# Kernel optimization log

Measured on AMD Instinct MI355X. Metric: run time of the kernel, lower is better.

## Reference

```python
import jax, jax.numpy as jnp
import numpy as np

HEAD_DIM = 64

def setup_inputs() -> dict:
    key = jax.random.key(0)
    k1, k2, k3, k4 = jax.random.split(key, 4)
    B, T, C, D = 8, 2048, 1024, HEAD_DIM
    x = jax.random.normal(k1, (B, T, C), dtype=jnp.float32)
    Wq = jax.random.normal(k2, (C, D), dtype=jnp.float32) * (1.0 / np.sqrt(C))
    Wk = jax.random.normal(k3, (C, D), dtype=jnp.float32) * (1.0 / np.sqrt(C))
    Wv = jax.random.normal(k4, (C, D), dtype=jnp.float32) * (1.0 / np.sqrt(C))
    return {"x": x, "Wq": Wq, "Wk": Wk, "Wv": Wv}

def reference(x, Wq, Wk, Wv):
    B, T, C = x.shape
    D = Wq.shape[1]
    q = jnp.einsum('btc,cd->btd', x, Wq)
    k = jnp.einsum('btc,cd->btd', x, Wk)
    v = jnp.einsum('btc,cd->btd', x, Wv)
    scale = 1.0 / jnp.sqrt(jnp.asarray(D, dtype=x.dtype))
    wei = jnp.einsum('bqd,bkd->bqk', q, k) * scale  # [B,T,T]
    causal = jnp.tril(jnp.ones((T, T), dtype=bool))
    wei = jnp.where(causal[None, :, :], wei, -jnp.inf)
    wei = jax.nn.softmax(wei, axis=-1)
    # dropout p=0.0 (eval) -> identity
    out = jnp.einsum('bqk,bkd->bqd', wei, v)  # [B,T,D]
    return out
```

## Files before the change

kernel.cpp:

```cpp
#include <hip/hip_runtime.h>
#include <hip/hip_bf16.h>


typedef __attribute__((ext_vector_type(8))) short short8;
typedef __attribute__((ext_vector_type(4))) float f32x4;

#define MFMA16(a, b, c) __builtin_amdgcn_mfma_f32_16x16x32_bf16((a), (b), (c), 0, 0, 0)

__device__ __forceinline__ unsigned short f2bf(float f) {
  unsigned int u = __builtin_bit_cast(unsigned int, f);
  unsigned int r = 0x7fffu + ((u >> 16) & 1u);
  return (unsigned short)((u + r) >> 16);
}

#define BATCH 8
#define SEQ   2048
#define CDIM  1024
#define DDIM  64
#define NTOK  (BATCH * SEQ)
#define LOG2E 1.44269504f

__global__ __launch_bounds__(256) void wt_kernel(const float* __restrict__ Wq,
                                                 const float* __restrict__ Wk,
                                                 const float* __restrict__ Wv,
                                                 unsigned short* __restrict__ WT) {
  int tid = blockIdx.x * 256 + threadIdx.x;
  int c    = tid & 63;
  int rest = tid >> 6;
  int k    = rest & 1023;
  int wi   = rest >> 10;
  const float* W = (wi == 0) ? Wq : ((wi == 1) ? Wk : Wv);
  float v = W[k * DDIM + c];
  if (wi == 0) v *= 0.125f * LOG2E;
  int row  = wi * 64 + c;
  int step = k >> 6;
  int col  = k & 63;
  size_t idx = (size_t)step * 12288 + (size_t)row * 64 +
               (size_t)(((col >> 3) ^ (row & 7)) * 8) + (col & 7);
  WT[idx] = f2bf(v);
}

__global__ __launch_bounds__(512) void proj_kernel(const float* __restrict__ x,
                                                   const unsigned short* __restrict__ WT,
                                                   unsigned short* __restrict__ qws,
                                                   unsigned short* __restrict__ kws,
                                                   unsigned short* __restrict__ vtws) {
  __shared__ __align__(16) unsigned short xs[2][32 * 64];
  __shared__ __align__(16) unsigned short wl[2][192 * 64];

  const int tid  = threadIdx.x;
  const int lane = tid & 63;
  const int w    = tid >> 6;
  const int wm   = w & 1;
  const int wn   = w >> 1;
  const int c16  = lane & 15;
  const int hi   = lane >> 4;
  const int n0   = blockIdx.x * 32;
  const bool xldr = (tid < 256);
  const int trow = (tid >> 3) & 31;
  const int kch  = tid & 7;

  f32x4 acc[3];
#pragma unroll
  for (int ct = 0; ct < 3; ++ct) acc[ct] = (f32x4){0.f, 0.f, 0.f, 0.f};

  const float* xbase = x + (size_t)(n0 + trow) * CDIM + kch * 8;
  const int xsw = trow * 64 + ((kch ^ (trow & 7)) * 8);

  const unsigned short* wsrc = WT + (size_t)w * 1536 + (size_t)lane * 8;
  auto stage_wt = [&](int step, int bufi) {
    const unsigned short* s = wsrc + (size_t)step * 12288;
    unsigned short* d = &wl[bufi][w * 1536];
#pragma unroll
    for (int j = 0; j < 3; ++j)
      __builtin_amdgcn_global_load_lds(
          (const __attribute__((address_space(1))) void*)(s + j * 512),
          (__attribute__((address_space(3))) void*)(d + j * 512), 16, 0, 0);
  };
  auto xstore = [&](f32x4 a, f32x4 b, int bufi) {
    short8 h;
#pragma unroll
    for (int j = 0; j < 4; ++j) { h[j] = (short)f2bf(a[j]); h[4 + j] = (short)f2bf(b[j]); }
    *reinterpret_cast<short8*>(&xs[bufi][xsw]) = h;
  };

  f32x4 xa1 = {0,0,0,0}, xb1 = xa1, xa2 = xa1, xb2 = xa1;
  if (xldr) {
    f32x4 a0 = *reinterpret_cast<const f32x4*>(xbase);
    f32x4 b0 = *reinterpret_cast<const f32x4*>(xbase + 4);
    xstore(a0, b0, 0);
    xa1 = *reinterpret_cast<const f32x4*>(xbase + 64);
    xb1 = *reinterpret_cast<const f32x4*>(xbase + 64 + 4);
  }
  stage_wt(0, 0);
  __syncthreads();

  int cur = 0;
  for (int st = 0; st < 16; ++st) {
    if (st + 2 < 16 && xldr) {
      xa2 = *reinterpret_cast<const f32x4*>(xbase + (st + 2) * 64);
      xb2 = *reinterpret_cast<const f32x4*>(xbase + (st + 2) * 64 + 4);
    }
    if (st + 1 < 16) stage_wt(st + 1, cur ^ 1);

    short8 bfrag[2];
    {
      int r = wm * 16 + c16;
#pragma unroll
      for (int f = 0; f < 2; ++f)
        bfrag[f] = *reinterpret_cast<const short8*>(
            &xs[cur][r * 64 + (((f * 4 + hi) ^ (r & 7)) * 8)]);
    }
#pragma unroll
    for (int ct = 0; ct < 3; ++ct) {
      int ra = (wn * 3 + ct) * 16 + c16;
#pragma unroll
      for (int f = 0; f < 2; ++f) {
        short8 af = *reinterpret_cast<const short8*>(
            &wl[cur][ra * 64 + (((f * 4 + hi) ^ (ra & 7)) * 8)]);
        acc[ct] = MFMA16(af, bfrag[f], acc[ct]);
      }
    }

    if (st + 1 < 16 && xldr) xstore(xa1, xb1, cur ^ 1);
    __syncthreads();
    xa1 = xa2; xb1 = xb2;
    cur ^= 1;
  }

  {
    const int token = n0 + wm * 16 + c16;
    const int b = token >> 11;
    const int t = token & 2047;
#pragma unroll
    for (int ct = 0; ct < 3; ++ct) {
      int cg = (wn * 3 + ct) * 16 + hi * 4;
      unsigned short h[4];
#pragma unroll
      for (int r = 0; r < 4; ++r) h[r] = f2bf(acc[ct][r]);
      if (cg < 64) {
        *reinterpret_cast<ushort4*>(qws + (size_t)token * DDIM + cg) =
            make_ushort4(h[0], h[1], h[2], h[3]);
      } else if (cg < 128) {
        *reinterpret_cast<ushort4*>(kws + (size_t)token * DDIM + (cg - 64)) =
            make_ushort4(h[0], h[1], h[2], h[3]);
      } else {
        int cv = cg - 128;
#pragma unroll
        for (int r = 0; r < 4; ++r)
          vtws[(size_t)(b * DDIM + cv + r) * SEQ + t] = h[r];
      }
    }
  }
}

__global__ __launch_bounds__(256) void attn_partial(const unsigned short* __restrict__ qws,
                                                    const unsigned short* __restrict__ kws,
                                                    const unsigned short* __restrict__ vtws,
                                                    float* __restrict__ po,
                                                    float* __restrict__ pml,
                                                    int MAXCH, int CHUNK) {
  __shared__ __align__(16) unsigned short kt[2][64 * 64];
  __shared__ __align__(16) unsigned short vt[2][64 * 64];
  __shared__ __align__(16) unsigned short pt[4][1024];

  const int id = blockIdx.x;
  const int b  = id & 7;
  const int qt = (id >> 3) & 31;
  const int ch = id >> 8;

  const int kv_end = qt * 64 + 64;
  const int kv0_ch = ch * CHUNK;
  if (kv0_ch >= kv_end) return;
  const int block_lim = min(kv0_ch + CHUNK, kv_end);
  const int nt = (block_lim - kv0_ch + 63) >> 6;

  const int tid  = threadIdx.x;
  const int lane = tid & 63;
  const int w    = tid >> 6;
  const int c    = lane & 15;
  const int hi   = lane >> 4;
  const int qr0  = qt * 64 + w * 16;
  const int q    = qr0 + c;
  const int kv_last = qr0 + 15;

  const unsigned short* qb = qws + (size_t)b * SEQ * DDIM;
  short8 aq0 = *reinterpret_cast<const short8*>(qb + (size_t)q * DDIM + hi * 8);
  short8 aq1 = *reinterpret_cast<const short8*>(qb + (size_t)q * DDIM + 32 + hi * 8);

  float m = -INFINITY, l = 0.f;
  f32x4 o[4];
#pragma unroll
  for (int dn = 0; dn < 4; ++dn) o[dn] = (f32x4){0.f, 0.f, 0.f, 0.f};

  unsigned short* pwv = pt[w];
  const unsigned short* kb = kws + (size_t)b * SEQ * DDIM;
  const unsigned short* vb = vtws + (size_t)b * DDIM * SEQ;

  auto stage_kv = [&](int bufi, int kv0) {
#pragma unroll
    for (int j = 0; j < 2; ++j) {
      int p   = w * 128 + j * 64 + lane;
      int row = p >> 3;
      int chk = (p & 7) ^ (row & 7);
      __builtin_amdgcn_global_load_lds(
          (const __attribute__((address_space(1))) void*)(kb + (size_t)(kv0 + row) * DDIM + chk * 8),
          (__attribute__((address_space(3))) void*)(&kt[bufi][w * 1024 + j * 512]), 16, 0, 0);
      __builtin_amdgcn_global_load_lds(
          (const __attribute__((address_space(1))) void*)(vb + (size_t)row * SEQ + kv0 + chk * 8),
          (__attribute__((address_space(3))) void*)(&vt[bufi][w * 1024 + j * 512]), 16, 0, 0);
    }
  };

  stage_kv(0, kv0_ch);
  asm volatile("s_waitcnt vmcnt(0)" ::: "memory");
  __builtin_amdgcn_s_barrier();

  int cur = 0;
  for (int t = 0; t < nt; ++t) {
    const int kv0 = kv0_ch + t * 64;
    if (t + 1 < nt) stage_kv(cur ^ 1, kv0 + 64);

    if (kv0 <= kv_last) {
      f32x4 s[4];
#pragma unroll
      for (int n = 0; n < 4; ++n) {
        if (kv0 + n * 16 > kv_last) {
          s[n] = (f32x4){-INFINITY, -INFINITY, -INFINITY, -INFINITY};
          continue;
        }
        const unsigned short* kr = &kt[cur][(n * 16 + c) * 64];
        short8 ka0 = *reinterpret_cast<const short8*>(kr + ((hi ^ (c & 7)) * 8));
        short8 ka1 = *reinterpret_cast<const short8*>(kr + (((4 + hi) ^ (c & 7)) * 8));
        f32x4 z = (f32x4){0.f, 0.f, 0.f, 0.f};
        z = MFMA16(ka0, aq0, z);
        s[n] = MFMA16(ka1, aq1, z);
      }

      if (kv0 + 63 > qr0) {
#pragma unroll
        for (int n = 0; n < 4; ++n)
#pragma unroll
          for (int r = 0; r < 4; ++r)
            if (kv0 + n * 16 + hi * 4 + r > q) s[n][r] = -INFINITY;
      }

      float mx = -INFINITY;
#pragma unroll
      for (int n = 0; n < 4; ++n)
        mx = fmaxf(mx, fmaxf(fmaxf(s[n][0], s[n][1]), fmaxf(s[n][2], s[n][3])));
      mx = fmaxf(mx, __shfl_xor(mx, 16, 64));
      mx = fmaxf(mx, __shfl_xor(mx, 32, 64));

      float nm = fmaxf(m, mx);
      float sc = __builtin_exp2f(m - nm);
      m = nm;

      float ssum = 0.f;
#pragma unroll
      for (int n = 0; n < 4; ++n) {
        float pv0 = __builtin_exp2f(s[n][0] - nm);
        float pv1 = __builtin_exp2f(s[n][1] - nm);
        float pv2 = __builtin_exp2f(s[n][2] - nm);
        float pv3 = __builtin_exp2f(s[n][3] - nm);
        ssum += (pv0 + pv1) + (pv2 + pv3);
        ushort4 h4 = make_ushort4(f2bf(pv0), f2bf(pv1), f2bf(pv2), f2bf(pv3));
        *reinterpret_cast<ushort4*>(
            pwv + (2 * n + (hi >> 1)) * 128 + c * 8 + (hi & 1) * 4) = h4;
      }
      ssum += __shfl_xor(ssum, 16, 64);
      ssum += __shfl_xor(ssum, 32, 64);
      l = l * sc + ssum;

#pragma unroll
      for (int dn = 0; dn < 4; ++dn) o[dn] *= sc;

      const int nf = (kv0 + 32 <= kv_last) ? 2 : 1;
      for (int f = 0; f < nf; ++f) {
        short8 bp = *reinterpret_cast<const short8*>(pwv + (f * 4 + hi) * 128 + c * 8);
#pragma unroll
        for (int dn = 0; dn < 4; ++dn) {
          const unsigned short* vr = &vt[cur][(dn * 16 + c) * 64];
          short8 va = *reinterpret_cast<const short8*>(vr + (((f * 4 + hi) ^ (c & 7)) * 8));
          o[dn] = MFMA16(va, bp, o[dn]);
        }
      }
    }

    if (t + 1 < nt) {
      asm volatile("s_waitcnt vmcnt(0)" ::: "memory");
      __builtin_amdgcn_s_barrier();
    }
    cur ^= 1;
  }

  float* pob = po + (((size_t)(b * 32 + qt) * MAXCH + ch) * 64 + w * 16 + c) * 64 + hi * 4;
#pragma unroll
  for (int dn = 0; dn < 4; ++dn)
    *reinterpret_cast<f32x4*>(pob + dn * 16) = o[dn];

  if (hi == 0) {
    *reinterpret_cast<float2*>(
        pml + (((size_t)(b * 32 + qt) * MAXCH + ch) * 64 + w * 16 + c) * 2) =
        make_float2(m, l);
  }
}

__global__ __launch_bounds__(256) void attn_combine(const float* __restrict__ po,
                                                    const float* __restrict__ pml,
                                                    float* __restrict__ out,
                                                    int MAXCH, int CHUNK) {
  const int id = blockIdx.x;
  const int b  = id & 7;
  const int qt = id >> 3;
  const int tid = threadIdx.x;
  const int row = tid >> 2;
  const int cg  = tid & 3;
  const int nch = min((qt * 64 + 64 + CHUNK - 1) / CHUNK, MAXCH);

  const size_t base = (size_t)(b * 32 + qt) * MAXCH;

  float mv0 = -INFINITY, mv1 = -INFINITY, mv2 = -INFINITY, mv3 = -INFINITY;
  float mv4 = -INFINITY, mv5 = -INFINITY, mv6 = -INFINITY, mv7 = -INFINITY;
  float lv0 = 0, lv1 = 0, lv2 = 0, lv3 = 0, lv4 = 0, lv5 = 0, lv6 = 0, lv7 = 0;
#define LOADML(i) if (i < nch) { \
    float2 t = *reinterpret_cast<const float2*>(pml + (base + i) * 128 + row * 2); \
    mv##i = t.x; lv##i = t.y; }
  LOADML(0) LOADML(1) LOADML(2) LOADML(3) LOADML(4) LOADML(5) LOADML(6) LOADML(7)
#undef LOADML

  float M = fmaxf(fmaxf(fmaxf(mv0, mv1), fmaxf(mv2, mv3)),
                  fmaxf(fmaxf(mv4, mv5), fmaxf(mv6, mv7)));

  float L = 0.f;
  f32x4 a0 = {0.f,0.f,0.f,0.f}, a1 = a0, a2 = a0, a3 = a0;
#define ACC(i) if (i < nch) { \
    float wgt = __builtin_exp2f(mv##i - M); \
    L += wgt * lv##i; \
    const float* p = po + (base + i) * 4096 + row * 64 + cg * 16; \
    a0 += wgt * *reinterpret_cast<const f32x4*>(p); \
    a1 += wgt * *reinterpret_cast<const f32x4*>(p + 4); \
    a2 += wgt * *reinterpret_cast<const f32x4*>(p + 8); \
    a3 += wgt * *reinterpret_cast<const f32x4*>(p + 12); }
  ACC(0) ACC(1) ACC(2) ACC(3) ACC(4) ACC(5) ACC(6) ACC(7)
#undef ACC

  float invL = 1.f / L;
  float* ob = out + ((size_t)b * SEQ + qt * 64 + row) * 64 + cg * 16;
  *reinterpret_cast<f32x4*>(ob)      = a0 * invL;
  *reinterpret_cast<f32x4*>(ob + 4)  = a1 * invL;
  *reinterpret_cast<f32x4*>(ob + 8)  = a2 * invL;
  *reinterpret_cast<f32x4*>(ob + 12) = a3 * invL;
}

extern "C" void kernel_launch(void* const* d_in, const int* in_sizes, int n_in,
                              void* d_out, int out_size, void* d_ws, size_t ws_size,
                              hipStream_t stream) {
  const float* x  = (const float*)d_in[0];
  const float* Wq = (const float*)d_in[1];
  const float* Wk = (const float*)d_in[2];
  const float* Wv = (const float*)d_in[3];
  float* out = (float*)d_out;

  unsigned short* qws  = (unsigned short*)d_ws;
  unsigned short* kws  = qws + (size_t)NTOK * DDIM;
  unsigned short* vtws = kws + (size_t)NTOK * DDIM;
  unsigned short* WT   = vtws + (size_t)NTOK * DDIM;
  size_t fixed_end = (size_t)NTOK * DDIM * 3 * 2 + 192 * 1024 * 2;

  int MAXCH = 1;
  {
    const int cand[4] = {8, 4, 2, 1};
    for (int i = 0; i < 4; ++i) {
      size_t need = fixed_end +
                    (size_t)cand[i] * (8ull * 32 * 64 * 64 * 4 + 8ull * 32 * 64 * 2 * 4);
      if (need <= ws_size) { MAXCH = cand[i]; break; }
    }
  }

  wt_kernel<<<768, 256, 0, stream>>>(Wq, Wk, Wv, WT);
  proj_kernel<<<NTOK / 32, 512, 0, stream>>>(x, WT, qws, kws, vtws);

  float* po  = (float*)((char*)d_ws + fixed_end);
  float* pml = po + (size_t)BATCH * 32 * MAXCH * 64 * 64;
  int CHUNK = SEQ / MAXCH;
  attn_partial<<<32 * MAXCH * BATCH, 256, 0, stream>>>(qws, kws, vtws, po, pml,
                                                       MAXCH, CHUNK);
  attn_combine<<<32 * BATCH, 256, 0, stream>>>(po, pml, out, MAXCH, CHUNK);
}
```

Baseline: 55.10 us.

## Load K/V fragments directly from global memory and reverse query-tile order

Removes the LDS double-buffered K/V staging and block barriers, so each wave loads its MFMA operand fragments straight from global memory (relying on L1/L2 caching), and loops only up to its own causal limit. It also reverses query-tile block order so the heaviest causal tiles launch first. This gets rid of barrier synchronisation and LDS traffic, and lets waves skip tiles independently. In exchange, each of the four waves re-reads the same K/V from global/L2 with no software prefetch, which raises cache traffic and can expose memory latency.

```diff
diff --git a/kernel.cpp b/kernel.cpp
--- a/kernel.cpp
+++ b/kernel.cpp
@@ -160,20 +160,17 @@
                                                     float* __restrict__ po,
                                                     float* __restrict__ pml,
                                                     int MAXCH, int CHUNK) {
-  __shared__ __align__(16) unsigned short kt[2][64 * 64];
-  __shared__ __align__(16) unsigned short vt[2][64 * 64];
   __shared__ __align__(16) unsigned short pt[4][1024];
 
   const int id = blockIdx.x;
   const int b  = id & 7;
-  const int qt = (id >> 3) & 31;
+  const int qt = 31 - ((id >> 3) & 31);
   const int ch = id >> 8;
 
   const int kv_end = qt * 64 + 64;
   const int kv0_ch = ch * CHUNK;
   if (kv0_ch >= kv_end) return;
   const int block_lim = min(kv0_ch + CHUNK, kv_end);
-  const int nt = (block_lim - kv0_ch + 63) >> 6;
 
   const int tid  = threadIdx.x;
   const int lane = tid & 63;
@@ -197,101 +194,81 @@
   const unsigned short* kb = kws + (size_t)b * SEQ * DDIM;
   const unsigned short* vb = vtws + (size_t)b * DDIM * SEQ;
 
-  auto stage_kv = [&](int bufi, int kv0) {
-#pragma unroll
-    for (int j = 0; j < 2; ++j) {
-      int p   = w * 128 + j * 64 + lane;
-      int row = p >> 3;
-      int chk = (p & 7) ^ (row & 7);
-      __builtin_amdgcn_global_load_lds(
-          (const __attribute__((address_space(1))) void*)(kb + (size_t)(kv0 + row) * DDIM + chk * 8),
-          (__attribute__((address_space(3))) void*)(&kt[bufi][w * 1024 + j * 512]), 16, 0, 0);
-      __builtin_amdgcn_global_load_lds(
-          (const __attribute__((address_space(1))) void*)(vb + (size_t)row * SEQ + kv0 + chk * 8),
-          (__attribute__((address_space(3))) void*)(&vt[bufi][w * 1024 + j * 512]), 16, 0, 0);
-    }
-  };
-
-  stage_kv(0, kv0_ch);
-  asm volatile("s_waitcnt vmcnt(0)" ::: "memory");
-  __builtin_amdgcn_s_barrier();
-
-  int cur = 0;
-  for (int t = 0; t < nt; ++t) {
-    const int kv0 = kv0_ch + t * 64;
-    if (t + 1 < nt) stage_kv(cur ^ 1, kv0 + 64);
-
-    if (kv0 <= kv_last) {
-      f32x4 s[4];
-#pragma unroll
-      for (int n = 0; n < 4; ++n) {
-        if (kv0 + n * 16 > kv_last) {
-          s[n] = (f32x4){-INFINITY, -INFINITY, -INFINITY, -INFINITY};
-          continue;
-        }
-        const unsigned short* kr = &kt[cur][(n * 16 + c) * 64];
-        short8 ka0 = *reinterpret_cast<const short8*>(kr + ((hi ^ (c & 7)) * 8));
-        short8 ka1 = *reinterpret_cast<const short8*>(kr + (((4 + hi) ^ (c & 7)) * 8));
+  const int lim = min(block_lim, kv_last + 1);
+
+  for (int kv0 = kv0_ch; kv0 < lim; kv0 += 64) {
+    const int nn = min(3, (kv_last - kv0) >> 4);
+
+    short8 ka[4][2];
+#pragma unroll
+    for (int n = 0; n < 4; ++n) {
+      if (n <= nn) {
+        const unsigned short* kr = kb + (size_t)(kv0 + n * 16 + c) * DDIM + hi * 8;
+        ka[n][0] = *reinterpret_cast<const short8*>(kr);
+        ka[n][1] = *reinterpret_cast<const short8*>(kr + 32);
+      }
+    }
+
+    f32x4 s[4];
+#pragma unroll
+    for (int n = 0; n < 4; ++n) {
+      if (n <= nn) {
         f32x4 z = (f32x4){0.f, 0.f, 0.f, 0.f};
-        z = MFMA16(ka0, aq0, z);
-        s[n] = MFMA16(ka1, aq1, z);
-      }
-
-      if (kv0 + 63 > qr0) {
-#pragma unroll
-        for (int n = 0; n < 4; ++n)
-#pragma unroll
-          for (int r = 0; r < 4; ++r)
-            if (kv0 + n * 16 + hi * 4 + r > q) s[n][r] = -INFINITY;
-      }
-
-      float mx = -INFINITY;
+        z = MFMA16(ka[n][0], aq0, z);
+        s[n] = MFMA16(ka[n][1], aq1, z);
+      } else {
+        s[n] = (f32x4){-INFINITY, -INFINITY, -INFINITY, -INFINITY};
+      }
+    }
+
+    if (kv0 + 63 > qr0) {
 #pragma unroll
       for (int n = 0; n < 4; ++n)
-        mx = fmaxf(mx, fmaxf(fmaxf(s[n][0], s[n][1]), fmaxf(s[n][2], s[n][3])));
-      mx = fmaxf(mx, __shfl_xor(mx, 16, 64));
-      mx = fmaxf(mx, __shfl_xor(mx, 32, 64));
-
-      float nm = fmaxf(m, mx);
-      float sc = __builtin_exp2f(m - nm);
-      m = nm;
-
-      float ssum = 0.f;
-#pragma unroll
-      for (int n = 0; n < 4; ++n) {
-        float pv0 = __builtin_exp2f(s[n][0] - nm);
-        float pv1 = __builtin_exp2f(s[n][1] - nm);
-        float pv2 = __builtin_exp2f(s[n][2] - nm);
-        float pv3 = __builtin_exp2f(s[n][3] - nm);
-        ssum += (pv0 + pv1) + (pv2 + pv3);
-        ushort4 h4 = make_ushort4(f2bf(pv0), f2bf(pv1), f2bf(pv2), f2bf(pv3));
-        *reinterpret_cast<ushort4*>(
-            pwv + (2 * n + (hi >> 1)) * 128 + c * 8 + (hi & 1) * 4) = h4;
-      }
-      ssum += __shfl_xor(ssum, 16, 64);
-      ssum += __shfl_xor(ssum, 32, 64);
-      l = l * sc + ssum;
-
-#pragma unroll
-      for (int dn = 0; dn < 4; ++dn) o[dn] *= sc;
-
-      const int nf = (kv0 + 32 <= kv_last) ? 2 : 1;
-      for (int f = 0; f < nf; ++f) {
-        short8 bp = *reinterpret_cast<const short8*>(pwv + (f * 4 + hi) * 128 + c * 8);
-#pragma unroll
-        for (int dn = 0; dn < 4; ++dn) {
-          const unsigned short* vr = &vt[cur][(dn * 16 + c) * 64];
-          short8 va = *reinterpret_cast<const short8*>(vr + (((f * 4 + hi) ^ (c & 7)) * 8));
-          o[dn] = MFMA16(va, bp, o[dn]);
-        }
-      }
-    }
-
-    if (t + 1 < nt) {
-      asm volatile("s_waitcnt vmcnt(0)" ::: "memory");
-      __builtin_amdgcn_s_barrier();
-    }
-    cur ^= 1;
+#pragma unroll
+        for (int r = 0; r < 4; ++r)
+          if (kv0 + n * 16 + hi * 4 + r > q) s[n][r] = -INFINITY;
+    }
+
+    float mx = -INFINITY;
+#pragma unroll
+    for (int n = 0; n < 4; ++n)
+      mx = fmaxf(mx, fmaxf(fmaxf(s[n][0], s[n][1]), fmaxf(s[n][2], s[n][3])));
+    mx = fmaxf(mx, __shfl_xor(mx, 16, 64));
+    mx = fmaxf(mx, __shfl_xor(mx, 32, 64));
+
+    float nm = fmaxf(m, mx);
+    float sc = __builtin_exp2f(m - nm);
+    m = nm;
+
+    float ssum = 0.f;
+#pragma unroll
+    for (int n = 0; n < 4; ++n) {
+      float pv0 = __builtin_exp2f(s[n][0] - nm);
+      float pv1 = __builtin_exp2f(s[n][1] - nm);
+      float pv2 = __builtin_exp2f(s[n][2] - nm);
+      float pv3 = __builtin_exp2f(s[n][3] - nm);
+      ssum += (pv0 + pv1) + (pv2 + pv3);
+      ushort4 h4 = make_ushort4(f2bf(pv0), f2bf(pv1), f2bf(pv2), f2bf(pv3));
+      *reinterpret_cast<ushort4*>(
+          pwv + (2 * n + (hi >> 1)) * 128 + c * 8 + (hi & 1) * 4) = h4;
+    }
+    ssum += __shfl_xor(ssum, 16, 64);
+    ssum += __shfl_xor(ssum, 32, 64);
+    l = l * sc + ssum;
+
+#pragma unroll
+    for (int dn = 0; dn < 4; ++dn) o[dn] *= sc;
+
+    const int nf = (kv0 + 32 <= kv_last) ? 2 : 1;
+    for (int f = 0; f < nf; ++f) {
+      short8 bp = *reinterpret_cast<const short8*>(pwv + (f * 4 + hi) * 128 + c * 8);
+#pragma unroll
+      for (int dn = 0; dn < 4; ++dn) {
+        short8 va = *reinterpret_cast<const short8*>(
+            vb + (size_t)(dn * 16 + c) * SEQ + kv0 + f * 32 + hi * 8);
+        o[dn] = MFMA16(va, bp, o[dn]);
+      }
+    }
   }
 
   float* pob = po + (((size_t)(b * 32 + qt) * MAXCH + ch) * 64 + w * 16 + c) * 64 + hi * 4;
```

Result: slower. 80.44 us (+46.0%).
